# Kernel optimization log

Measured on AMD Instinct MI355X. Metric: run time of the kernel, lower is better.

Reference implementation:

```python
import jax, jax.numpy as jnp
import numpy as np

B, S, T = 64, 24, 96
V, E, H, A = 32000, 256, 512, 512


def setup_inputs() -> dict:
    key = jax.random.key(0)
    ks = jax.random.split(key, 16)
    captions = jax.random.randint(ks[0], (B, S, T), 0, V)
    lengths = jax.random.randint(ks[1], (B, S), 1, T + 1)
    lengths = lengths.at[0].set(T)  # ensure per-sentence max length == T (matches dynamic seq_len_k)
    update_masks = jnp.arange(T)[None, None, :] < lengths[:, :, None]  # [B,S,T] bool prefix mask
    p = lambda k, shp: jax.random.normal(k, shp, dtype=jnp.float32) * 0.05
    return dict(
        captions=captions, update_masks=update_masks,
        embed_W=p(ks[2], (V, E)),
        w_Wih=p(ks[3], (4 * H, E)), w_Whh=p(ks[4], (4 * H, H)),
        w_bih=p(ks[5], (4 * H,)), w_bhh=p(ks[6], (4 * H,)),
        s_Wih=p(ks[7], (4 * H, H)), s_Whh=p(ks[8], (4 * H, H)),
        s_bih=p(ks[9], (4 * H,)), s_bhh=p(ks[10], (4 * H,)),
        wa_Wk=p(ks[11], (A, H)), wa_Wv=p(ks[12], (1, A)),
        sa_Wk=p(ks[13], (A, H)), sa_Wv=p(ks[14], (1, A)),
    )


def _lstm_cell(x, h, c, Wih, Whh, bih, bhh):
    # torch.nn.LSTMCell gate order: i, f, g, o
    g = x @ Wih.T + bih + h @ Whh.T + bhh
    i, f, gg, o = jnp.split(g, 4, axis=-1)
    c2 = jax.nn.sigmoid(f) * c + jax.nn.sigmoid(i) * jnp.tanh(gg)
    h2 = jax.nn.sigmoid(o) * jnp.tanh(c2)
    return h2, c2


def _attn(k, Wk, Wv):
    # SelfAttention: softmax(affine(tanh(affine_k(k)))) pooled context
    z = (jnp.tanh(k @ Wk.T) @ Wv.T)[..., 0]          # [B,L]
    alpha = jax.nn.softmax(z, axis=1)
    ctx = jnp.einsum('blh,bl->bh', k, alpha)
    return ctx, alpha


def reference(captions, update_masks, embed_W, w_Wih, w_Whh, w_bih, w_bhh,
              s_Wih, s_Whh, s_bih, s_bhh, wa_Wk, wa_Wv, sa_Wk, sa_Wv):
    emb = embed_W[captions]                            # [B,S,T,E]
    bsz = captions.shape[0]
    zeros = jnp.zeros((bsz, H), jnp.float32)

    def sent_step(carry, ins):
        sh, sc, wh, wc = carry
        emb_k, m_k = ins                               # [B,T,E], [B,T]

        def word_step(c2, inp):
            wh_, wc_ = c2
            x, m = inp                                 # [B,E], [B] bool
            nh, nc = _lstm_cell(x, wh_, wc_, w_Wih, w_Whh, w_bih, w_bhh)
            m1 = m[:, None]
            # masked state update; inactive positions store 0 in word_hs
            return (jnp.where(m1, nh, wh_), jnp.where(m1, nc, wc_)), jnp.where(m1, nh, 0.0)

        (wh, wc), hs = jax.lax.scan(word_step, (wh, wc),
                                    (emb_k.transpose(1, 0, 2), m_k.T))
        word_hs = hs.transpose(1, 0, 2)                # [B,T,H]
        ctx, _ = _attn(word_hs, wa_Wk, wa_Wv)
        sh, sc = _lstm_cell(ctx, sh, sc, s_Wih, s_Whh, s_bih, s_bhh)
        return (sh, sc, wh, wc), sh

    _, sent_hs = jax.lax.scan(sent_step, (zeros, zeros, zeros, zeros),
                              (emb.transpose(1, 0, 2, 3), update_masks.transpose(1, 0, 2)))
    sent_hs = sent_hs.transpose(1, 0, 2)               # [B,S,H]
    context, alpha = _attn(sent_hs, sa_Wk, sa_Wv)
    return context, alpha
```

## Files before the change

### kernel.cpp

```cpp
#include <hip/hip_runtime.h>
#include <hip/hip_cooperative_groups.h>
#include <math.h>

namespace cg = cooperative_groups;

constexpr int kB = 64, kS = 24, kT = 96, kE = 256, kH = 512, kA = 512;
constexpr int NWG = 256, NTH = 512;
constexpr int NG = 8, GWG = 32, GB = 8;
constexpr int WHP = 516;
constexpr int HSP = 580;
constexpr int EMP = 264;
constexpr int EMB0 = 4640;
constexpr int ATP = 516;

constexpr int OFF_PUB = 0;
constexpr int OFF_SH  = OFF_PUB + 2 * NG * GWG * 128;
constexpr int OFF_HS  = OFF_SH + 2 * kB * kH;
constexpr int OFF_Z   = OFF_HS + kB * kT * kH;
constexpr int OFF_CTX = OFF_Z + kB * kT;
constexpr int OFF_SHS = OFF_CTX + kB * kH;
constexpr int OFF_Z2  = OFF_SHS + kB * kS * kH;
constexpr int OFF_FLG = (OFF_Z2 + kB * kS + 31) & ~31;

typedef float f4v __attribute__((ext_vector_type(4)));

__device__ __forceinline__ float sigmoidf(float x) { return 1.0f / (1.0f + expf(-x)); }
__device__ __forceinline__ float dot4(float4 a, float4 b) {
  return a.x * b.x + a.y * b.y + a.z * b.z + a.w * b.w;
}
__device__ __forceinline__ float2 aload2(const float* p) {
  unsigned long long u = __hip_atomic_load((const unsigned long long*)p,
                                           __ATOMIC_RELAXED, __HIP_MEMORY_SCOPE_AGENT);
  union { unsigned long long u; float2 f; } cv; cv.u = u;
  return cv.f;
}
__device__ __forceinline__ float aload1(const float* p) {
  return __hip_atomic_load(p, __ATOMIC_RELAXED, __HIP_MEMORY_SCOPE_AGENT);
}
__device__ __forceinline__ void astore(float* p, float v) {
  __hip_atomic_store(p, v, __ATOMIC_RELAXED, __HIP_MEMORY_SCOPE_AGENT);
}
__device__ __forceinline__ unsigned aloadu(const unsigned* p) {
  return __hip_atomic_load(p, __ATOMIC_RELAXED, __HIP_MEMORY_SCOPE_AGENT);
}
__device__ __forceinline__ void astoreu(unsigned* p, unsigned v) {
  __hip_atomic_store(p, v, __ATOMIC_RELAXED, __HIP_MEMORY_SCOPE_AGENT);
}
__device__ __forceinline__ unsigned l2_loadu(const unsigned* p) {
  unsigned r;
  asm volatile("global_load_dword %0, %1, off sc0\n\ts_waitcnt vmcnt(0)"
               : "=v"(r) : "v"(p) : "memory");
  return r;
}
__device__ __forceinline__ float l2_load1(const float* p) {
  float r;
  asm volatile("global_load_dword %0, %1, off sc0\n\ts_waitcnt vmcnt(0)"
               : "=v"(r) : "v"(p) : "memory");
  return r;
}
__device__ __forceinline__ float2 l2_load2(const float* p) {
  float2 r;
  asm volatile("global_load_dwordx2 %0, %1, off sc0\n\ts_waitcnt vmcnt(0)"
               : "=v"(r) : "v"(p) : "memory");
  return r;
}
__device__ __forceinline__ void l2_load8(const float* p, f4v& a, f4v& b) {
  asm volatile("global_load_dwordx4 %0, %2, off sc0\n\t"
               "global_load_dwordx4 %1, %2, off offset:16 sc0\n\t"
               "s_waitcnt vmcnt(0)"
               : "=&v"(a), "=&v"(b) : "v"(p) : "memory");
}
__device__ __forceinline__ void l2_load4s(const float* p0, const float* p1,
                                          const float* p2, const float* p3,
                                          float& r0, float& r1, float& r2, float& r3) {
  asm volatile("global_load_dword %0, %4, off sc0\n\t"
               "global_load_dword %1, %5, off sc0\n\t"
               "global_load_dword %2, %6, off sc0\n\t"
               "global_load_dword %3, %7, off sc0\n\t"
               "s_waitcnt vmcnt(0)"
               : "=&v"(r0), "=&v"(r1), "=&v"(r2), "=&v"(r3)
               : "v"(p0), "v"(p1), "v"(p2), "v"(p3) : "memory");
}
__device__ __forceinline__ void l2_atomic_inc(unsigned* p) {
  unsigned one = 1u;
  asm volatile("global_atomic_add %0, %1, off" :: "v"(p), "v"(one) : "memory");
}

__global__ __launch_bounds__(NTH, 2) void ha_kernel(
    const int* __restrict__ captions, const int* __restrict__ masks,
    const float* __restrict__ embed_W,
    const float* __restrict__ w_Wih, const float* __restrict__ w_Whh,
    const float* __restrict__ w_bih, const float* __restrict__ w_bhh,
    const float* __restrict__ s_Wih, const float* __restrict__ s_Whh,
    const float* __restrict__ s_bih, const float* __restrict__ s_bhh,
    const float* __restrict__ wa_Wk, const float* __restrict__ wa_Wv,
    const float* __restrict__ sa_Wk, const float* __restrict__ sa_Wv,
    float* __restrict__ out, float* __restrict__ ws) {
  cg::grid_group grid = cg::this_grid();
  const int g = blockIdx.x, tid = threadIdx.x;
  const int jj = tid >> 6;
  const int c = tid & 63;
  const int half = (tid >> 5) & 1;
  const int c2 = tid & 31;
  const int ks = jj * 2 + half;

  float* pub = ws + OFF_PUB;
  float* sh_buf = ws + OFF_SH;
  float* hs_buf = ws + OFF_HS;
  float* z_buf = ws + OFF_Z;
  float* ctx_ws = ws + OFF_CTX;
  float* sent_hs = ws + OFF_SHS;
  float* z2_buf = ws + OFF_Z2;
  unsigned* flags = (unsigned*)(ws + OFF_FLG);
  unsigned* cntp = flags + 8192;
  unsigned* tflagA = flags + 8448;
  unsigned* tdataA = flags + 8704;
  unsigned* verdA = flags + 8960;

  __shared__ __align__(16) float whh_s[64 * WHP];
  __shared__ __align__(16) float uni[6752];
  __shared__ float bias_s[64];
  __shared__ float c_s[16][8], hown_s[16][8], sc_s[16][8];
  __shared__ unsigned mbits[24];
  __shared__ float soft_s[96], red_s[96];
  __shared__ int ibuf[4];

  {
    int idx = g * NTH + tid;
    if (idx < 2 * kB * kH) sh_buf[idx] = 0.f;
  }
  if (g == 0)
    for (int idx = tid; idx < 9216; idx += NTH) flags[idx] = 0u;
  grid.sync();

  if (tid == 0) {
    unsigned xcc;
    asm volatile("s_getreg_b32 %0, hwreg(20, 0, 32)" : "=s"(xcc));
    xcc &= 7u;
    unsigned slot = atomicAdd(&cntp[xcc * 32], 1u);
    ibuf[0] = (int)xcc; ibuf[1] = (int)slot;
  }
  grid.sync();
  __syncthreads();
  const int myxcc = ibuf[0], myslot = ibuf[1];
  unsigned cnts[8]; int px[9]; px[0] = 0;
  for (int x = 0; x < 8; ++x) { cnts[x] = aloadu(&cntp[x * 32]); px[x + 1] = px[x] + (int)cnts[x]; }
  const int rank = px[myxcc] + myslot;
  const int grp = rank >> 5, r = rank & 31;
  const int B0 = GB * grp;
  bool pure = false;
  for (int x = 0; x < 8; ++x)
    if (px[x] <= grp * 32 && grp * 32 + 32 <= px[x + 1]) pure = true;
  const bool cand = pure && (cnts[myxcc] <= 40u);
  unsigned* myflag = &flags[(grp * GWG + r) * 32];

  auto g_row = [&](int cc) { return (cc >> 4) * kH + 16 * r + (cc & 15); };

  unsigned n = 0;
  {
    unsigned* tf = &tflagA[grp * 32];
    unsigned* td = &tdataA[grp * 32];
    int ok = 0;
    if (cand && r == 0 && tid == 0) {
      *td = 0xC0FFEEu;
      asm volatile("s_waitcnt vmcnt(0)" ::: "memory");
      l2_atomic_inc(tf);
    }
    if (cand && tid == 0) {
      for (int it = 0; it < 4096; ++it) {
        if (l2_loadu(tf) >= 1u) { ok = (l2_loadu(td) == 0xC0FFEEu); break; }
        __builtin_amdgcn_s_sleep(2);
      }
    }
    if (tid == 0) {
      astoreu(&verdA[grp * 32 + r], ok ? 1u : 0u);
      asm volatile("s_waitcnt vmcnt(0)" ::: "memory");
      atomicAdd(myflag, 1u);
    }
    n = 1;
    if (tid < GWG) {
      while (aloadu(&flags[(grp * GWG + tid) * 32]) < 1u) __builtin_amdgcn_s_sleep(2);
    }
    __syncthreads();
    if (tid < GWG) red_s[tid] = (float)aloadu(&verdA[grp * 32 + tid]);
    __syncthreads();
    if (tid == 0) {
      int all = 1;
      for (int i = 0; i < GWG; ++i) all &= (red_s[i] != 0.f);
      ibuf[2] = all;
    }
    __syncthreads();
  }
  const bool l2m = (ibuf[2] != 0);

  auto mstore1 = [&](float* p, float v) { if (l2m) *p = v; else astore(p, v); };
  auto mload1 = [&](const float* p) { return l2m ? l2_load1(p) : aload1(p); };
  auto mload2 = [&](const float* p) { return l2m ? l2_load2(p) : aload2(p); };
  auto mload8 = [&](const float* p, f4v& a, f4v& b) {
    if (l2m) l2_load8(p, a, b);
    else {
      float2 t0 = aload2(p), t1 = aload2(p + 2), t2 = aload2(p + 4), t3 = aload2(p + 6);
      a = f4v{t0.x, t0.y, t1.x, t1.y}; b = f4v{t2.x, t2.y, t3.x, t3.y};
    }
  };
  auto mload4s = [&](const float* p0, const float* p1, const float* p2, const float* p3,
                     float& r0, float& r1, float& r2, float& r3) {
    if (l2m) l2_load4s(p0, p1, p2, p3, r0, r1, r2, r3);
    else { r0 = aload1(p0); r1 = aload1(p1); r2 = aload1(p2); r3 = aload1(p3); }
  };
  auto arrive = [&]() {
    __syncthreads();
    if (tid == 0) { if (l2m) l2_atomic_inc(myflag); else atomicAdd(myflag, 1u); }
  };
  auto wait = [&](unsigned nn) {
    if (tid < GWG) {
      const unsigned* fp = &flags[(grp * GWG + tid) * 32];
      if (l2m) { while (l2_loadu(fp) < nn) __builtin_amdgcn_s_sleep(1); }
      else     { while (aloadu(fp) < nn)   __builtin_amdgcn_s_sleep(1); }
    }
    __syncthreads();
  };

  for (int idx = tid; idx < 64 * kH; idx += NTH) {
    const int cr = idx >> 9, kk = idx & 511;
    whh_s[cr * WHP + 4 * (((kk >> 2) + 4 * (cr & 1)) & 127) + (kk & 3)] =
        w_Whh[(size_t)g_row(cr) * kH + kk];
  }
  if (tid < 64) bias_s[tid] = w_bih[g_row(tid)] + w_bhh[g_row(tid)];
  if (tid < 128) {
    c_s[tid >> 3][tid & 7] = 0.f; hown_s[tid >> 3][tid & 7] = 0.f; sc_s[tid >> 3][tid & 7] = 0.f;
  }
  for (int idx = tid; idx < 6752; idx += NTH) uni[idx] = 0.f;
  __syncthreads();

  auto stage_hst_pub = [&](const float* slab) {
    const int lin = tid * 8, rsm = lin >> 7, rem = lin & 127;
    const int b2 = rem >> 4, kk = (rsm << 4) | (rem & 15);
    f4v a, b4; mload8(slab + lin, a, b4);
    const int ho = kk + 4 * (kk >> 5);
    *(f4v*)&uni[b2 * HSP + ho] = a;
    *(f4v*)&uni[b2 * HSP + ho + 4] = b4;
  };
  auto stage_hst_lin = [&](const float* src) {
    const int lin = tid * 8, b2 = lin >> 9, kk = lin & 511;
    f4v a, b4; mload8(src + lin, a, b4);
    const int ho = kk + 4 * (kk >> 5);
    *(f4v*)&uni[b2 * HSP + ho] = a;
    *(f4v*)&uni[b2 * HSP + ho + 4] = b4;
  };
  auto stage_emb = [&](int s2, int t2) {
    const int b2 = tid >> 6, ch = tid & 63;
    const int cap = captions[((B0 + b2) * kS + s2) * kT + t2];
    const float4 v = *(const float4*)&embed_W[(size_t)cap * kE + 4 * ch];
    *(float4*)&uni[EMB0 + b2 * EMP + 4 * ch] = v;
  };
  float xp0[8], xp1[8];
  auto calc_xp = [&]() {
    const float* wrA = w_Wih + (size_t)g_row(c2) * kE + 16 * ks;
    const float* wrB = w_Wih + (size_t)g_row(c2 + 32) * kE + 16 * ks;
    const float* eb = &uni[EMB0 + 16 * ks];
#pragma unroll
    for (int b2 = 0; b2 < 8; ++b2) { xp0[b2] = 0.f; xp1[b2] = 0.f; }
#pragma unroll
    for (int v = 0; v < 4; ++v) {
      const float4 wA = *(const float4*)&wrA[4 * v];
      const float4 wB = *(const float4*)&wrB[4 * v];
#pragma unroll
      for (int b2 = 0; b2 < 8; ++b2) {
        const float4 ev = *(const float4*)&eb[b2 * EMP + 4 * v];
        xp0[b2] += dot4(wA, ev);
        xp1[b2] += dot4(wB, ev);
      }
    }
  };

  stage_emb(0, 0);
  __syncthreads();
  calc_xp();

  int gstep = 0;
  for (int s = 0; s < kS; ++s) {
    if (tid < 24) {
      const int b2 = tid / 3, w2 = tid % 3;
      unsigned bits = 0u;
      const int base = ((B0 + b2) * kS + s) * kT + 32 * w2;
      for (int j = 0; j < 32; ++j) bits |= (masks[base + j] ? 1u : 0u) << j;
      mbits[b2 * 3 + w2] = bits;
    }
    if (s > 0) stage_hst_pub(pub + ((size_t)((gstep & 1) * NG + grp)) * 4096);
    __syncthreads();

    for (int t = 0; t < kT; ++t, ++gstep) {
      float* pubw = pub + ((size_t)(((gstep + 1) & 1) * NG + grp)) * 4096;

      float acc0[8], acc1[8];
#pragma unroll
      for (int b2 = 0; b2 < 8; ++b2) { acc0[b2] = xp0[b2]; acc1[b2] = xp1[b2]; }
      {
        const int swc = 4 * (c2 & 1);
        const float* w0 = &whh_s[c2 * WHP];
        const float* w1 = &whh_s[(c2 + 32) * WHP];
#pragma unroll
        for (int u = 0; u < 8; ++u) {
          const int q = 8 * ks + u;
          const float4 wv0 = *(const float4*)&w0[4 * ((q + swc) & 127)];
          const float4 wv1 = *(const float4*)&w1[4 * ((q + swc) & 127)];
          const int hoff = 4 * q + 4 * (q >> 3);
#pragma unroll
          for (int b2 = 0; b2 < 8; ++b2) {
            const float4 hv = *(const float4*)&uni[b2 * HSP + hoff];
            acc0[b2] += dot4(wv0, hv);
            acc1[b2] += dot4(wv1, hv);
          }
        }
      }
      __syncthreads();
#pragma unroll
      for (int b2 = 0; b2 < 8; ++b2) {
        const float t0 = acc0[b2] + __shfl_xor(acc0[b2], 32);
        const float t1 = acc1[b2] + __shfl_xor(acc1[b2], 32);
        uni[jj * HSP + (c2 + 32 * half) * 9 + b2] = half ? t1 : t0;
      }
      __syncthreads();
      float hsv = 0.f;
      if (tid < 128) {
        const int hcl = tid >> 3, b2 = tid & 7;
        float gg4[4];
#pragma unroll
        for (int g2 = 0; g2 < 4; ++g2) {
          const int cc = g2 * 16 + hcl;
          float sum = bias_s[cc];
#pragma unroll
          for (int j = 0; j < 8; ++j) sum += uni[j * HSP + cc * 9 + b2];
          gg4[g2] = sum;
        }
        const float cold = c_s[hcl][b2];
        const float c2v = sigmoidf(gg4[1]) * cold + sigmoidf(gg4[0]) * tanhf(gg4[2]);
        const float h2 = sigmoidf(gg4[3]) * tanhf(c2v);
        const int m = (mbits[b2 * 3 + (t >> 5)] >> (t & 31)) & 1;
        const float cn = m ? c2v : cold;
        const float hn = m ? h2 : hown_s[hcl][b2];
        c_s[hcl][b2] = cn; hown_s[hcl][b2] = hn;
        mstore1(&pubw[r * 128 + b2 * 16 + hcl], hn);
        hsv = m ? h2 : 0.f;
      }
      ++n;
      arrive();
      if (tid < 128) {
        const int hcl = tid >> 3, b2 = tid & 7;
        mstore1(&hs_buf[((size_t)(B0 + b2) * kT + t) * kH + 16 * r + hcl], hsv);
      }
      int ns = s, nt = t + 1; bool have = true;
      if (nt == kT) { nt = 0; ns = s + 1; if (ns == kS) have = false; }
      if (have) stage_emb(ns, nt);
      __syncthreads();
      if (have) calc_xp();
      wait(n);
      stage_hst_pub(pubw);
      __syncthreads();
    }

    ++n; arrive(); wait(n);

    {
      const int ab = r >> 2, t0 = (r & 3) * 24;
      const int bg = B0 + ab;
      for (int halfp = 0; halfp < 2; ++halfp) {
        const int tb = t0 + halfp * 12;
        for (int idx = tid; idx < 12 * 256; idx += NTH) {
          const int pp = idx >> 8, hh2 = (idx & 255) * 2;
          float2 v = mload2(&hs_buf[((size_t)bg * kT + tb + pp) * kH + hh2]);
          *(float2*)&uni[pp * ATP + hh2] = v;
        }
        __syncthreads();
        float dacc[12];
#pragma unroll
        for (int p = 0; p < 12; ++p) dacc[p] = 0.f;
        const float4* __restrict__ wk = (const float4*)(wa_Wk + (size_t)tid * kH);
        for (int k = 0; k < kH / 4; ++k) {
          const float4 w = wk[k];
#pragma unroll
          for (int p = 0; p < 12; ++p)
            dacc[p] += dot4(w, *(const float4*)&uni[p * ATP + 4 * k]);
        }
        const float wv = wa_Wv[tid];
        const int ln = tid & 63, wid = tid >> 6;
#pragma unroll
        for (int p = 0; p < 12; ++p) {
          float v = wv * tanhf(dacc[p]);
          v += __shfl_down(v, 32); v += __shfl_down(v, 16); v += __shfl_down(v, 8);
          v += __shfl_down(v, 4);  v += __shfl_down(v, 2);  v += __shfl_down(v, 1);
          if (ln == 0) red_s[wid * 12 + p] = v;
        }
        __syncthreads();
        if (tid < 12) {
          float sum = 0.f;
#pragma unroll
          for (int w = 0; w < 8; ++w) sum += red_s[w * 12 + tid];
          mstore1(&z_buf[bg * kT + tb + tid], sum);
        }
        __syncthreads();
      }
    }
    ++n; arrive(); wait(n);

    if (r < GB) {
      const int b2 = B0 + r;
      if (tid < kT) soft_s[tid] = mload1(&z_buf[b2 * kT + tid]);
      __syncthreads();
      float mx = -1e30f;
      for (int i = 0; i < kT; ++i) mx = fmaxf(mx, soft_s[i]);
      float den = 0.f;
      for (int i = 0; i < kT; ++i) den += expf(soft_s[i] - mx);
      __syncthreads();
      if (tid < kT) soft_s[tid] = expf(soft_s[tid] - mx) / den;
      __syncthreads();
      {
        const int h0 = tid;
        float a0 = 0.f, a1 = 0.f, a2 = 0.f, a3 = 0.f;
        for (int tt = 0; tt < kT; tt += 4) {
          const float* p = &hs_buf[((size_t)b2 * kT + tt) * kH + h0];
          float v0, v1, v2, v3;
          mload4s(p, p + kH, p + 2 * kH, p + 3 * kH, v0, v1, v2, v3);
          a0 += soft_s[tt + 0] * v0;
          a1 += soft_s[tt + 1] * v1;
          a2 += soft_s[tt + 2] * v2;
          a3 += soft_s[tt + 3] * v3;
        }
        mstore1(&ctx_ws[b2 * kH + h0], (a0 + a1) + (a2 + a3));
      }
    }
    ++n; arrive(); wait(n);

    {
      float acc[8];
#pragma unroll
      for (int b2 = 0; b2 < 8; ++b2) acc[b2] = 0.f;
      stage_hst_lin(ctx_ws + B0 * kH);
      __syncthreads();
      {
        const float* wA = s_Wih + (size_t)g_row(c) * kH + 64 * jj;
#pragma unroll 8
        for (int u = 0; u < 16; ++u) {
          const float4 w = *(const float4*)&wA[4 * u];
          const int q = 16 * jj + u;
          const int hoff = 4 * q + 4 * (q >> 3);
#pragma unroll
          for (int b2 = 0; b2 < 8; ++b2)
            acc[b2] += dot4(w, *(const float4*)&uni[b2 * HSP + hoff]);
        }
      }
      __syncthreads();
      stage_hst_lin(sh_buf + (s & 1) * kB * kH + B0 * kH);
      __syncthreads();
      {
        const float* wB = s_Whh + (size_t)g_row(c) * kH + 64 * jj;
#pragma unroll 8
        for (int u = 0; u < 16; ++u) {
          const float4 w = *(const float4*)&wB[4 * u];
          const int q = 16 * jj + u;
          const int hoff = 4 * q + 4 * (q >> 3);
#pragma unroll
          for (int b2 = 0; b2 < 8; ++b2)
            acc[b2] += dot4(w, *(const float4*)&uni[b2 * HSP + hoff]);
        }
      }
      __syncthreads();
#pragma unroll
      for (int b2 = 0; b2 < 8; ++b2) uni[jj * HSP + c * 9 + b2] = acc[b2];
      __syncthreads();
      if (tid < 128) {
        const int hcl = tid >> 3, b2 = tid & 7;
        float gg4[4];
#pragma unroll
        for (int g2 = 0; g2 < 4; ++g2) {
          const int cc = g2 * 16 + hcl;
          const int row = g_row(cc);
          float sum = s_bih[row] + s_bhh[row];
#pragma unroll
          for (int j = 0; j < 8; ++j) sum += uni[j * HSP + cc * 9 + b2];
          gg4[g2] = sum;
        }
        const float c2v = sigmoidf(gg4[1]) * sc_s[hcl][b2] + sigmoidf(gg4[0]) * tanhf(gg4[2]);
        const float h2 = sigmoidf(gg4[3]) * tanhf(c2v);
        sc_s[hcl][b2] = c2v;
        const int col = 16 * r + hcl;
        mstore1(&sh_buf[((s + 1) & 1) * kB * kH + (B0 + b2) * kH + col], h2);
        mstore1(&sent_hs[((size_t)(B0 + b2) * kS + s) * kH + col], h2);
      }
    }
    ++n; arrive(); wait(n);
  }

  {
    const int pair0 = r * 6;
    for (int idx = tid; idx < 6 * 256; idx += NTH) {
      const int pp = idx >> 8, hh2 = (idx & 255) * 2;
      const int pr = pair0 + pp;
      float2 v = mload2(&sent_hs[((size_t)(B0 + pr / kS) * kS + pr % kS) * kH + hh2]);
      *(float2*)&uni[pp * ATP + hh2] = v;
    }
    __syncthreads();
    float dacc[6];
#pragma unroll
    for (int p = 0; p < 6; ++p) dacc[p] = 0.f;
    const float4* __restrict__ wk = (const float4*)(sa_Wk + (size_t)tid * kH);
    for (int k = 0; k < kH / 4; ++k) {
      const float4 w = wk[k];
#pragma unroll
      for (int p = 0; p < 6; ++p)
        dacc[p] += dot4(w, *(const float4*)&uni[p * ATP + 4 * k]);
    }
    const float wv = sa_Wv[tid];
    const int ln = tid & 63, wid = tid >> 6;
#pragma unroll
    for (int p = 0; p < 6; ++p) {
      float v = wv * tanhf(dacc[p]);
      v += __shfl_down(v, 32); v += __shfl_down(v, 16); v += __shfl_down(v, 8);
      v += __shfl_down(v, 4);  v += __shfl_down(v, 2);  v += __shfl_down(v, 1);
      if (ln == 0) red_s[wid * 6 + p] = v;
    }
    __syncthreads();
    if (tid < 6) {
      float sum = 0.f;
#pragma unroll
      for (int w = 0; w < 8; ++w) sum += red_s[w * 6 + tid];
      mstore1(&z2_buf[B0 * kS + pair0 + tid], sum);
    }
  }
  ++n; arrive(); wait(n);

  if (r < GB) {
    const int b2 = B0 + r;
    if (tid < kS) soft_s[tid] = mload1(&z2_buf[b2 * kS + tid]);
    __syncthreads();
    float mx = -1e30f;
    for (int i = 0; i < kS; ++i) mx = fmaxf(mx, soft_s[i]);
    float den = 0.f;
    for (int i = 0; i < kS; ++i) den += expf(soft_s[i] - mx);
    __syncthreads();
    if (tid < kS) {
      const float al = expf(soft_s[tid] - mx) / den;
      soft_s[tid] = al;
      out[kB * kH + b2 * kS + tid] = al;
    }
    __syncthreads();
    {
      const int h0 = tid;
      float acc2 = 0.f;
      for (int s2 = 0; s2 < kS; ++s2)
        acc2 += soft_s[s2] * mload1(&sent_hs[((size_t)b2 * kS + s2) * kH + h0]);
      out[b2 * kH + h0] = acc2;
    }
  }
}

extern "C" void kernel_launch(void* const* d_in, const int* in_sizes, int n_in,
                              void* d_out, int out_size, void* d_ws, size_t ws_size,
                              hipStream_t stream) {
  (void)in_sizes; (void)n_in; (void)out_size; (void)ws_size;
  const int* captions = (const int*)d_in[0];
  const int* masks = (const int*)d_in[1];
  const float* embed_W = (const float*)d_in[2];
  const float* w_Wih = (const float*)d_in[3];
  const float* w_Whh = (const float*)d_in[4];
  const float* w_bih = (const float*)d_in[5];
  const float* w_bhh = (const float*)d_in[6];
  const float* s_Wih = (const float*)d_in[7];
  const float* s_Whh = (const float*)d_in[8];
  const float* s_bih = (const float*)d_in[9];
  const float* s_bhh = (const float*)d_in[10];
  const float* wa_Wk = (const float*)d_in[11];
  const float* wa_Wv = (const float*)d_in[12];
  const float* sa_Wk = (const float*)d_in[13];
  const float* sa_Wv = (const float*)d_in[14];
  float* out = (float*)d_out;
  float* ws = (float*)d_ws;

  void* args[] = {&captions, &masks, &embed_W, &w_Wih, &w_Whh, &w_bih, &w_bhh,
                  &s_Wih, &s_Whh, &s_bih, &s_bhh, &wa_Wk, &wa_Wv, &sa_Wk, &sa_Wv,
                  &out, &ws};
  hipLaunchCooperativeKernel((void*)ha_kernel, dim3(NWG), dim3(NTH), args, 0, stream);
}
```

Baseline: 22.89 ms.

## Retile word-LSTM recurrent matvec to 4 gate rows by 4 batches per thread

```diff
diff --git a/kernel.cpp b/kernel.cpp
--- a/kernel.cpp
+++ b/kernel.cpp
@@ -84,6 +84,9 @@
 __device__ __forceinline__ void l2_atomic_inc(unsigned* p) {
   unsigned one = 1u;
   asm volatile("global_atomic_add %0, %1, off" :: "v"(p), "v"(one) : "memory");
+}
+__device__ __forceinline__ void nt_store1(float* p, float v) {
+  asm volatile("global_store_dword %0, %1, off nt" :: "v"(p), "v"(v) : "memory");
 }
 
 __global__ __launch_bounds__(NTH, 2) void ha_kernel(
@@ -100,9 +103,10 @@
   const int g = blockIdx.x, tid = threadIdx.x;
   const int jj = tid >> 6;
   const int c = tid & 63;
-  const int half = (tid >> 5) & 1;
-  const int c2 = tid & 31;
-  const int ks = jj * 2 + half;
+  const int q4 = tid & 15;
+  const int bh = (tid >> 4) & 1;
+  const int ksl = tid >> 5;
+  const int m32 = (tid >> 5) & 1;
 
   float* pub = ws + OFF_PUB;
   float* sh_buf = ws + OFF_SH;
@@ -194,6 +198,7 @@
   const bool l2m = (ibuf[2] != 0);
 
   auto mstore1 = [&](float* p, float v) { if (l2m) *p = v; else astore(p, v); };
+  auto ntstore = [&](float* p, float v) { if (l2m) nt_store1(p, v); else astore(p, v); };
   auto mload1 = [&](const float* p) { return l2m ? l2_load1(p) : aload1(p); };
   auto mload2 = [&](const float* p) { return l2m ? l2_load2(p) : aload2(p); };
   auto mload8 = [&](const float* p, f4v& a, f4v& b) {
@@ -209,6 +214,7 @@
     else { r0 = aload1(p0); r1 = aload1(p1); r2 = aload1(p2); r3 = aload1(p3); }
   };
   auto arrive = [&]() {
+    asm volatile("s_waitcnt vmcnt(0)" ::: "memory");
     __syncthreads();
     if (tid == 0) { if (l2m) l2_atomic_inc(myflag); else atomicAdd(myflag, 1u); }
   };
@@ -254,29 +260,39 @@
     const float4 v = *(const float4*)&embed_W[(size_t)cap * kE + 4 * ch];
     *(float4*)&uni[EMB0 + b2 * EMP + 4 * ch] = v;
   };
-  float xp0[8], xp1[8];
-  auto calc_xp = [&]() {
-    const float* wrA = w_Wih + (size_t)g_row(c2) * kE + 16 * ks;
-    const float* wrB = w_Wih + (size_t)g_row(c2 + 32) * kE + 16 * ks;
-    const float* eb = &uni[EMB0 + 16 * ks];
-#pragma unroll
-    for (int b2 = 0; b2 < 8; ++b2) { xp0[b2] = 0.f; xp1[b2] = 0.f; }
-#pragma unroll
-    for (int v = 0; v < 4; ++v) {
-      const float4 wA = *(const float4*)&wrA[4 * v];
-      const float4 wB = *(const float4*)&wrB[4 * v];
-#pragma unroll
-      for (int b2 = 0; b2 < 8; ++b2) {
-        const float4 ev = *(const float4*)&eb[b2 * EMP + 4 * v];
-        xp0[b2] += dot4(wA, ev);
-        xp1[b2] += dot4(wB, ev);
+
+  float acc[4][4];
+  auto calc_xp = [&](int s2, int t2) {
+    int caps[4];
+#pragma unroll
+    for (int bi = 0; bi < 4; ++bi)
+      caps[bi] = captions[((B0 + 4 * bh + bi) * kS + s2) * kT + t2];
+#pragma unroll
+    for (int i = 0; i < 4; ++i)
+#pragma unroll
+      for (int bi = 0; bi < 4; ++bi) acc[i][bi] = 0.f;
+    const int e0 = 16 * ksl;
+    const float* eb = &uni[EMB0 + 4 * bh * EMP + e0];
+#pragma unroll
+    for (int u = 0; u < 4; ++u) {
+      float4 wv0 = *(const float4*)&w_Wih[(size_t)g_row(q4)      * kE + e0 + 4 * u];
+      float4 wv1 = *(const float4*)&w_Wih[(size_t)g_row(q4 + 16) * kE + e0 + 4 * u];
+      float4 wv2 = *(const float4*)&w_Wih[(size_t)g_row(q4 + 32) * kE + e0 + 4 * u];
+      float4 wv3 = *(const float4*)&w_Wih[(size_t)g_row(q4 + 48) * kE + e0 + 4 * u];
+#pragma unroll
+      for (int bi = 0; bi < 4; ++bi) {
+        const float4 xv = *(const float4*)&eb[bi * EMP + 4 * u];
+        acc[0][bi] += dot4(wv0, xv);
+        acc[1][bi] += dot4(wv1, xv);
+        acc[2][bi] += dot4(wv2, xv);
+        acc[3][bi] += dot4(wv3, xv);
       }
     }
   };
 
   stage_emb(0, 0);
   __syncthreads();
-  calc_xp();
+  calc_xp(0, 0);
 
   int gstep = 0;
   for (int s = 0; s < kS; ++s) {
@@ -293,33 +309,43 @@
     for (int t = 0; t < kT; ++t, ++gstep) {
       float* pubw = pub + ((size_t)(((gstep + 1) & 1) * NG + grp)) * 4096;
 
-      float acc0[8], acc1[8];
-#pragma unroll
-      for (int b2 = 0; b2 < 8; ++b2) { acc0[b2] = xp0[b2]; acc1[b2] = xp1[b2]; }
       {
-        const int swc = 4 * (c2 & 1);
-        const float* w0 = &whh_s[c2 * WHP];
-        const float* w1 = &whh_s[(c2 + 32) * WHP];
+        const int swc = 4 * (q4 & 1);
+        const float* w0 = &whh_s[(q4     ) * WHP];
+        const float* w1 = &whh_s[(q4 + 16) * WHP];
+        const float* w2 = &whh_s[(q4 + 32) * WHP];
+        const float* w3 = &whh_s[(q4 + 48) * WHP];
+        const float* hb = &uni[4 * bh * HSP];
 #pragma unroll
         for (int u = 0; u < 8; ++u) {
-          const int q = 8 * ks + u;
-          const float4 wv0 = *(const float4*)&w0[4 * ((q + swc) & 127)];
-          const float4 wv1 = *(const float4*)&w1[4 * ((q + swc) & 127)];
+          const int q = 8 * ksl + u;
+          const int off = 4 * ((q + swc) & 127);
+          const float4 wv0 = *(const float4*)&w0[off];
+          const float4 wv1 = *(const float4*)&w1[off];
+          const float4 wv2 = *(const float4*)&w2[off];
+          const float4 wv3 = *(const float4*)&w3[off];
           const int hoff = 4 * q + 4 * (q >> 3);
 #pragma unroll
-          for (int b2 = 0; b2 < 8; ++b2) {
-            const float4 hv = *(const float4*)&uni[b2 * HSP + hoff];
-            acc0[b2] += dot4(wv0, hv);
-            acc1[b2] += dot4(wv1, hv);
+          for (int bi = 0; bi < 4; ++bi) {
+            const float4 hv = *(const float4*)&hb[bi * HSP + hoff];
+            acc[0][bi] += dot4(wv0, hv);
+            acc[1][bi] += dot4(wv1, hv);
+            acc[2][bi] += dot4(wv2, hv);
+            acc[3][bi] += dot4(wv3, hv);
           }
         }
       }
       __syncthreads();
 #pragma unroll
-      for (int b2 = 0; b2 < 8; ++b2) {
-        const float t0 = acc0[b2] + __shfl_xor(acc0[b2], 32);
-        const float t1 = acc1[b2] + __shfl_xor(acc1[b2], 32);
-        uni[jj * HSP + (c2 + 32 * half) * 9 + b2] = half ? t1 : t0;
+      for (int ih = 0; ih < 2; ++ih) {
+        const int col = q4 + 16 * ih + 32 * m32;
+#pragma unroll
+        for (int bi = 0; bi < 4; ++bi) {
+          const float own  = m32 ? acc[2 + ih][bi] : acc[ih][bi];
+          const float send = m32 ? acc[ih][bi]     : acc[2 + ih][bi];
+          const float v = own + __shfl_xor(send, 32);
+          uni[jj * HSP + col * 9 + 4 * bh + bi] = v;
+        }
       }
       __syncthreads();
       float hsv = 0.f;
@@ -348,13 +374,13 @@
       arrive();
       if (tid < 128) {
         const int hcl = tid >> 3, b2 = tid & 7;
-        mstore1(&hs_buf[((size_t)(B0 + b2) * kT + t) * kH + 16 * r + hcl], hsv);
+        ntstore(&hs_buf[((size_t)(B0 + b2) * kT + t) * kH + 16 * r + hcl], hsv);
       }
       int ns = s, nt = t + 1; bool have = true;
       if (nt == kT) { nt = 0; ns = s + 1; if (ns == kS) have = false; }
       if (have) stage_emb(ns, nt);
       __syncthreads();
-      if (have) calc_xp();
+      if (have) calc_xp(ns, nt);
       wait(n);
       stage_hst_pub(pubw);
       __syncthreads();
@@ -433,9 +459,9 @@
     ++n; arrive(); wait(n);
 
     {
-      float acc[8];
-#pragma unroll
-      for (int b2 = 0; b2 < 8; ++b2) acc[b2] = 0.f;
+      float sacc[8];
+#pragma unroll
+      for (int b2 = 0; b2 < 8; ++b2) sacc[b2] = 0.f;
       stage_hst_lin(ctx_ws + B0 * kH);
       __syncthreads();
       {
@@ -447,7 +473,7 @@
           const int hoff = 4 * q + 4 * (q >> 3);
 #pragma unroll
           for (int b2 = 0; b2 < 8; ++b2)
-            acc[b2] += dot4(w, *(const float4*)&uni[b2 * HSP + hoff]);
+            sacc[b2] += dot4(w, *(const float4*)&uni[b2 * HSP + hoff]);
         }
       }
       __syncthreads();
@@ -462,12 +488,12 @@
           const int hoff = 4 * q + 4 * (q >> 3);
 #pragma unroll
           for (int b2 = 0; b2 < 8; ++b2)
-            acc[b2] += dot4(w, *(const float4*)&uni[b2 * HSP + hoff]);
-        }
-      }
-      __syncthreads();
-#pragma unroll
-      for (int b2 = 0; b2 < 8; ++b2) uni[jj * HSP + c * 9 + b2] = acc[b2];
+            sacc[b2] += dot4(w, *(const float4*)&uni[b2 * HSP + hoff]);
+        }
+      }
+      __syncthreads();
+#pragma unroll
+      for (int b2 = 0; b2 < 8; ++b2) uni[jj * HSP + c * 9 + b2] = sacc[b2];
       __syncthreads();
       if (tid < 128) {
         const int hcl = tid >> 3, b2 = tid & 7;
@@ -486,7 +512,7 @@
         sc_s[hcl][b2] = c2v;
         const int col = 16 * r + hcl;
         mstore1(&sh_buf[((s + 1) & 1) * kB * kH + (B0 + b2) * kH + col], h2);
-        mstore1(&sent_hs[((size_t)(B0 + b2) * kS + s) * kH + col], h2);
+        ntstore(&sent_hs[((size_t)(B0 + b2) * kS + s) * kH + col], h2);
       }
     }
     ++n; arrive(); wait(n);
```

Result: slower. 64.23 ms (+180.5%).
